# Optimization experiments

Hardware: AMD Instinct MI355X
Metric: run time of the kernel (lower is better)

Reference implementation:

```python
import jax, jax.numpy as jnp
import numpy as np

N_NODES, N_EDGES, D, H, G = 50000, 800000, 128, 128, 2048
EPS_BN = 1e-5


def _bn(x, g, b, m, v):
    # inference-mode BatchNorm1d
    return (x - m) * jax.lax.rsqrt(v + EPS_BN) * g + b


def _gin_mlp(h, w1, b1, g1, be1, m1, v1, w2, b2, g2, be2, m2, v2):
    h = jax.nn.relu(_bn(h @ w1 + b1, g1, be1, m1, v1))
    return jax.nn.relu(_bn(h @ w2 + b2, g2, be2, m2, v2))


def _gin(x, src, dst, *mlp_params):
    # GINConv with eps=0: MLP(x_i + sum_{j->i} x_j)
    agg = jax.ops.segment_sum(x[src], dst, num_segments=x.shape[0])
    return _gin_mlp(x + agg, *mlp_params)


def setup_inputs() -> dict:
    key = jax.random.key(0)
    ks = jax.random.split(key, 16)
    inp = {
        'x': jax.random.normal(ks[0], (N_NODES, D), dtype=jnp.float32),
        'edge_index': jax.random.randint(ks[1], (2, N_EDGES), 0, N_NODES, dtype=jnp.int64),
        'batch': jnp.sort(jax.random.randint(ks[2], (N_NODES,), 0, G, dtype=jnp.int64)),
    }
    def lin(k, fin, fout):
        return jax.random.normal(k, (fin, fout), dtype=jnp.float32) * (1.0 / np.sqrt(fin))
    # conv1 MLP
    inp.update(w11=lin(ks[3], D, H), b11=jnp.zeros((H,)), g11=jnp.ones((H,)), be11=jnp.zeros((H,)), m11=jnp.zeros((H,)), v11=jnp.ones((H,)))
    inp.update(w12=lin(ks[4], H, H), b12=jnp.zeros((H,)), g12=jnp.ones((H,)), be12=jnp.zeros((H,)), m12=jnp.zeros((H,)), v12=jnp.ones((H,)))
    # conv2 MLP
    inp.update(w21=lin(ks[5], H, H), b21=jnp.zeros((H,)), g21=jnp.ones((H,)), be21=jnp.zeros((H,)), m21=jnp.zeros((H,)), v21=jnp.ones((H,)))
    inp.update(w22=lin(ks[6], H, H), b22=jnp.zeros((H,)), g22=jnp.ones((H,)), be22=jnp.zeros((H,)), m22=jnp.zeros((H,)), v22=jnp.ones((H,)))
    # classifier
    inp.update(wc1=lin(ks[7], H, 64), bc1=jnp.zeros((64,)), gc1=jnp.ones((64,)), bec1=jnp.zeros((64,)), mc1=jnp.zeros((64,)), vc1=jnp.ones((64,)))
    inp.update(wc2=lin(ks[8], 64, 2), bc2=jnp.zeros((2,)))
    return inp


def reference(x, edge_index, batch,
              w11, b11, g11, be11, m11, v11, w12, b12, g12, be12, m12, v12,
              w21, b21, g21, be21, m21, v21, w22, b22, g22, be22, m22, v22,
              wc1, bc1, gc1, bec1, mc1, vc1, wc2, bc2):
    src, dst = edge_index[0], edge_index[1]
    out1 = _gin(x, src, dst, w11, b11, g11, be11, m11, v11, w12, b12, g12, be12, m12, v12)
    # F.relu on already-ReLU'd output is a no-op but kept for fidelity
    out1 = jax.nn.relu(out1)
    out2 = _gin(out1, src, dst, w21, b21, g21, be21, m21, v21, w22, b22, g22, be22, m22, v22)
    out2 = jax.nn.relu(out2)
    # global mean pool over graph ids
    sums = jax.ops.segment_sum(out2, batch, num_segments=G)
    cnt = jax.ops.segment_sum(jnp.ones((out2.shape[0],), out2.dtype), batch, num_segments=G)
    pooled = sums / jnp.maximum(cnt, 1.0)[:, None]
    # classifier (dropout = identity in eval)
    h = jax.nn.relu(_bn(pooled @ wc1 + bc1, gc1, bec1, mc1, vc1))
    logits = h @ wc2 + bc2
    return logits
```

## Files before the change

### kernel.cpp

```cpp
#include <hip/hip_runtime.h>

#define NN 50000
#define NE 800000
#define DD 128
#define GG 2048
#define EPS 1e-5f
#define NBUK 196
#define CHUNK 4096
#define CAP 5120
#define CVTB 3125

typedef __attribute__((ext_vector_type(8))) short short8;
typedef __attribute__((ext_vector_type(4))) float floatx4;

__device__ __forceinline__ ushort f2b(float f) {
  uint u = __float_as_uint(f);
  uint r = ((u >> 16) & 1u) + 0x7fffu;
  return (ushort)((u + r) >> 16);
}
__device__ __forceinline__ float b2f(ushort h) {
  return __uint_as_float(((uint)h) << 16);
}
__device__ __forceinline__ float blo(uint u) { return __uint_as_float(u << 16); }
__device__ __forceinline__ float bhi(uint u) { return __uint_as_float(u & 0xffff0000u); }

__global__ __launch_bounds__(256) void k_pre(
    const float* __restrict__ W11, const float* __restrict__ W12,
    const float* __restrict__ W21, const float* __restrict__ W22,
    const float* __restrict__ b11, const float* __restrict__ g11,
    const float* __restrict__ be11, const float* __restrict__ m11,
    const float* __restrict__ v11,
    const float* __restrict__ b12, const float* __restrict__ g12,
    const float* __restrict__ be12, const float* __restrict__ m12,
    const float* __restrict__ v12,
    const float* __restrict__ b21, const float* __restrict__ g21,
    const float* __restrict__ be21, const float* __restrict__ m21,
    const float* __restrict__ v21,
    const float* __restrict__ b22, const float* __restrict__ g22,
    const float* __restrict__ be22, const float* __restrict__ m22,
    const float* __restrict__ v22,
    ushort* __restrict__ Wb, float* __restrict__ albb,
    int* __restrict__ buk_cnt) {
  int t = threadIdx.x;
  int b = blockIdx.x;
  if (b == 64) {
    buk_cnt[t] = 0;
    if (t < DD) {
      float a;
      a = g11[t] * rsqrtf(v11[t] + EPS);
      albb[0 * DD + t] = a;
      albb[1 * DD + t] = (b11[t] - m11[t]) * a + be11[t];
      a = g12[t] * rsqrtf(v12[t] + EPS);
      albb[2 * DD + t] = a;
      albb[3 * DD + t] = (b12[t] - m12[t]) * a + be12[t];
      a = g21[t] * rsqrtf(v21[t] + EPS);
      albb[4 * DD + t] = a;
      albb[5 * DD + t] = (b21[t] - m21[t]) * a + be21[t];
      a = g22[t] * rsqrtf(v22[t] + EPS);
      albb[6 * DD + t] = a;
      albb[7 * DD + t] = (b22[t] - m22[t]) * a + be22[t];
    }
    return;
  }
  const float* Ws[4] = {W11, W12, W21, W22};
  int widx = b >> 4;
  int idx = (b & 15) * 256 + t;
  int c = idx >> 5;
  int k0 = (idx & 31) * 4;
  const float* W = Ws[widx];
  ushort4 p;
  p.x = f2b(W[(k0 + 0) * DD + c]);
  p.y = f2b(W[(k0 + 1) * DD + c]);
  p.z = f2b(W[(k0 + 2) * DD + c]);
  p.w = f2b(W[(k0 + 3) * DD + c]);
  *(ushort4*)&Wb[(size_t)widx * DD * DD + c * DD + (k0 ^ ((c & 7) << 3))] = p;
}

__global__ __launch_bounds__(256) void k_binC(const float4* __restrict__ x,
                                              short8* __restrict__ xb,
                                              const int* __restrict__ ei,
                                              int* __restrict__ buk_cnt,
                                              uint* __restrict__ buk_pairs) {
  __shared__ int hist[256];
  __shared__ int gbase[256];
  __shared__ int lcur[256];
  int t = threadIdx.x;
  if (blockIdx.x < CVTB) {
    int i = blockIdx.x * 256 + t;
    float4 a = x[2 * i], c = x[2 * i + 1];
    short8 v;
    v[0] = (short)f2b(a.x); v[1] = (short)f2b(a.y);
    v[2] = (short)f2b(a.z); v[3] = (short)f2b(a.w);
    v[4] = (short)f2b(c.x); v[5] = (short)f2b(c.y);
    v[6] = (short)f2b(c.z); v[7] = (short)f2b(c.w);
    xb[i] = v;
    return;
  }
  int blk = blockIdx.x - CVTB;
  int e0 = blk * CHUNK;
  int nE = min(CHUNK, NE - e0);
  hist[t] = 0;
  lcur[t] = 0;
  gbase[t] = 0;
  __syncthreads();
  uint pk[16];
#pragma unroll
  for (int i = 0; i < 16; ++i) {
    int off = i * 256 + t;
    if (off < nE) {
      int e = e0 + off;
      int s = ei[e], d = ei[NE + e];
      int b = d >> 8;
      pk[i] = ((uint)b << 24) | ((uint)(d & 255) << 16) | (uint)s;
      atomicAdd(&hist[b], 1);
    } else {
      pk[i] = 0xffffffffu;
    }
  }
  __syncthreads();
  if (t < NBUK && hist[t] > 0) gbase[t] = atomicAdd(&buk_cnt[t], hist[t]);
  __syncthreads();
#pragma unroll
  for (int i = 0; i < 16; ++i) {
    if (pk[i] != 0xffffffffu) {
      int b = pk[i] >> 24;
      int lo = atomicAdd(&lcur[b], 1);
      int off = gbase[b] + lo;
      if (off < CAP) buk_pairs[(size_t)b * CAP + off] = pk[i];
    }
  }
}

__global__ __launch_bounds__(256) void k_bfill(const uint* __restrict__ buk_pairs,
                                               const int* __restrict__ buk_cnt,
                                               int* __restrict__ row_ptr,
                                               int* __restrict__ csr_src) {
  __shared__ int sc[256];
  __shared__ int deg[256];
  __shared__ int pos[256];
  int b = blockIdx.x, t = threadIdx.x;
  int c = (t < NBUK) ? min(buk_cnt[t], CAP) : 0;
  sc[t] = c;
  __syncthreads();
  int s1 = c;
  for (int off = 1; off < 256; off <<= 1) {
    int o = (t >= off) ? sc[t - off] : 0;
    __syncthreads();
    s1 += o;
    sc[t] = s1;
    __syncthreads();
  }
  int beg = (b == 0) ? 0 : sc[b - 1];
  int cnt = sc[b] - beg;
  const uint* src = buk_pairs + (size_t)b * CAP;
  deg[t] = 0;
  __syncthreads();
  for (int i = t; i < cnt; i += 256) {
    atomicAdd(&deg[(src[i] >> 16) & 255], 1);
  }
  __syncthreads();
  int d = deg[t];
  int sum = d;
  pos[t] = sum;
  __syncthreads();
  for (int off = 1; off < 256; off <<= 1) {
    int o = (t >= off) ? pos[t - off] : 0;
    __syncthreads();
    sum += o;
    pos[t] = sum;
    __syncthreads();
  }
  int myStart = beg + sum - d;
  int node = b * 256 + t;
  if (node < NN) row_ptr[node] = myStart;
  if (node == NN - 1) row_ptr[NN] = NE;
  __syncthreads();
  pos[t] = myStart;
  __syncthreads();
  for (int i = t; i < cnt; i += 256) {
    uint p = src[i];
    int lo = atomicAdd(&pos[(p >> 16) & 255], 1);
    csr_src[lo] = (int)(p & 0xffffu);
  }
}

__global__ __launch_bounds__(256) void k_agg(const uint* __restrict__ X,
                                             const int* __restrict__ row_ptr,
                                             const int* __restrict__ csr_src,
                                             uint* __restrict__ out) {
  int node = (blockIdx.x * 256 + threadIdx.x) >> 6;
  if (node >= NN) return;
  int lane = threadIdx.x & 63;
  uint s0 = X[(size_t)node * 64 + lane];
  float ax = blo(s0), ay = bhi(s0);
  int beg = row_ptr[node], end = row_ptr[node + 1];
  for (int i = beg; i < end; i += 64) {
    int idx = i + lane;
    int my = (idx < end) ? __builtin_nontemporal_load(csr_src + idx) : 0;
    int cnt = min(64, end - i);
    int j = 0;
    for (; j + 8 <= cnt; j += 8) {
      int n0 = __shfl(my, j + 0);
      int n1 = __shfl(my, j + 1);
      int n2 = __shfl(my, j + 2);
      int n3 = __shfl(my, j + 3);
      int n4 = __shfl(my, j + 4);
      int n5 = __shfl(my, j + 5);
      int n6 = __shfl(my, j + 6);
      int n7 = __shfl(my, j + 7);
      uint v0 = X[(size_t)n0 * 64 + lane];
      uint v1 = X[(size_t)n1 * 64 + lane];
      uint v2 = X[(size_t)n2 * 64 + lane];
      uint v3 = X[(size_t)n3 * 64 + lane];
      uint v4 = X[(size_t)n4 * 64 + lane];
      uint v5 = X[(size_t)n5 * 64 + lane];
      uint v6 = X[(size_t)n6 * 64 + lane];
      uint v7 = X[(size_t)n7 * 64 + lane];
      ax += blo(v0); ay += bhi(v0);
      ax += blo(v1); ay += bhi(v1);
      ax += blo(v2); ay += bhi(v2);
      ax += blo(v3); ay += bhi(v3);
      ax += blo(v4); ay += bhi(v4);
      ax += blo(v5); ay += bhi(v5);
      ax += blo(v6); ay += bhi(v6);
      ax += blo(v7); ay += bhi(v7);
    }
    for (; j + 4 <= cnt; j += 4) {
      int n0 = __shfl(my, j + 0);
      int n1 = __shfl(my, j + 1);
      int n2 = __shfl(my, j + 2);
      int n3 = __shfl(my, j + 3);
      uint v0 = X[(size_t)n0 * 64 + lane];
      uint v1 = X[(size_t)n1 * 64 + lane];
      uint v2 = X[(size_t)n2 * 64 + lane];
      uint v3 = X[(size_t)n3 * 64 + lane];
      ax += blo(v0); ay += bhi(v0);
      ax += blo(v1); ay += bhi(v1);
      ax += blo(v2); ay += bhi(v2);
      ax += blo(v3); ay += bhi(v3);
    }
    for (; j < cnt; ++j) {
      int s = __shfl(my, j);
      uint v = X[(size_t)s * 64 + lane];
      ax += blo(v);
      ay += bhi(v);
    }
  }
  out[(size_t)node * 64 + lane] = (uint)f2b(ax) | ((uint)f2b(ay) << 16);
}

__global__ __launch_bounds__(256) void k_mlp(const ushort* __restrict__ A,
                                             const ushort* __restrict__ Wb1,
                                             const ushort* __restrict__ Wb2,
                                             const float* __restrict__ albb,
                                             ushort* __restrict__ out) {
  __shared__ ushort Wt[DD * DD];
  __shared__ ushort mid[64 * DD];
  __shared__ float al1[DD], bb1[DD], al2[DD], bb2[DD];
  int t = threadIdx.x;
  for (int ii = t; ii < 2048; ii += 256) ((short8*)Wt)[ii] = ((const short8*)Wb1)[ii];
  if (t < DD) {
    al1[t] = albb[0 * DD + t];
    bb1[t] = albb[1 * DD + t];
    al2[t] = albb[2 * DD + t];
    bb2[t] = albb[3 * DD + t];
  }
  int w = t >> 6, l = t & 63;
  int lr = l & 15, lg = l >> 4;
  int rowBase = blockIdx.x * 64 + w * 16;
  int arow = min(rowBase + lr, NN - 1);
  const short8* Ar = (const short8*)(A + (size_t)arow * DD);
  short8 a0 = Ar[0 * 4 + lg];
  short8 a1 = Ar[1 * 4 + lg];
  short8 a2 = Ar[2 * 4 + lg];
  short8 a3 = Ar[3 * 4 + lg];
  __syncthreads();

  int mrowb = w * 16;
#pragma unroll
  for (int ct = 0; ct < 8; ++ct) {
    int c = ct * 16 + lr;
    int sw = (c & 7) << 3;
    const ushort* wr = Wt + c * DD;
    short8 b0 = *(const short8*)(wr + ((0 * 32 + lg * 8) ^ sw));
    short8 b1 = *(const short8*)(wr + ((1 * 32 + lg * 8) ^ sw));
    short8 b2 = *(const short8*)(wr + ((2 * 32 + lg * 8) ^ sw));
    short8 b3 = *(const short8*)(wr + ((3 * 32 + lg * 8) ^ sw));
    floatx4 acc = {0.f, 0.f, 0.f, 0.f};
    acc = __builtin_amdgcn_mfma_f32_16x16x32_bf16(a0, b0, acc, 0, 0, 0);
    acc = __builtin_amdgcn_mfma_f32_16x16x32_bf16(a1, b1, acc, 0, 0, 0);
    acc = __builtin_amdgcn_mfma_f32_16x16x32_bf16(a2, b2, acc, 0, 0, 0);
    acc = __builtin_amdgcn_mfma_f32_16x16x32_bf16(a3, b3, acc, 0, 0, 0);
    float alc = al1[c], bbc = bb1[c];
#pragma unroll
    for (int reg = 0; reg < 4; ++reg) {
      int row = mrowb + lg * 4 + reg;
      mid[row * DD + (c ^ ((row & 7) << 3))] = f2b(fmaxf(acc[reg] * alc + bbc, 0.f));
    }
  }
  __syncthreads();

  int mr = mrowb + lr;
  int msw = (mr & 7) << 3;
  const ushort* mrp = mid + mr * DD;
  short8 c0 = *(const short8*)(mrp + ((0 * 32 + lg * 8) ^ msw));
  short8 c1 = *(const short8*)(mrp + ((1 * 32 + lg * 8) ^ msw));
  short8 c2 = *(const short8*)(mrp + ((2 * 32 + lg * 8) ^ msw));
  short8 c3 = *(const short8*)(mrp + ((3 * 32 + lg * 8) ^ msw));
  for (int ii = t; ii < 2048; ii += 256) ((short8*)Wt)[ii] = ((const short8*)Wb2)[ii];
  __syncthreads();

#pragma unroll
  for (int ct = 0; ct < 8; ++ct) {
    int c = ct * 16 + lr;
    int sw = (c & 7) << 3;
    const ushort* wr = Wt + c * DD;
    short8 b0 = *(const short8*)(wr + ((0 * 32 + lg * 8) ^ sw));
    short8 b1 = *(const short8*)(wr + ((1 * 32 + lg * 8) ^ sw));
    short8 b2 = *(const short8*)(wr + ((2 * 32 + lg * 8) ^ sw));
    short8 b3 = *(const short8*)(wr + ((3 * 32 + lg * 8) ^ sw));
    floatx4 acc = {0.f, 0.f, 0.f, 0.f};
    acc = __builtin_amdgcn_mfma_f32_16x16x32_bf16(c0, b0, acc, 0, 0, 0);
    acc = __builtin_amdgcn_mfma_f32_16x16x32_bf16(c1, b1, acc, 0, 0, 0);
    acc = __builtin_amdgcn_mfma_f32_16x16x32_bf16(c2, b2, acc, 0, 0, 0);
    acc = __builtin_amdgcn_mfma_f32_16x16x32_bf16(c3, b3, acc, 0, 0, 0);
    float alc = al2[c], bbc = bb2[c];
#pragma unroll
    for (int reg = 0; reg < 4; ++reg) {
      int r = rowBase + lg * 4 + reg;
      if (r < NN) {
        out[(size_t)r * DD + c] = f2b(fmaxf(acc[reg] * alc + bbc, 0.f));
      }
    }
  }
}

__device__ __forceinline__ int lb(const int* __restrict__ a, int n, int v) {
  int lo = 0, hi = n;
  while (lo < hi) {
    int mid = (lo + hi) >> 1;
    if (a[mid] < v) lo = mid + 1;
    else hi = mid;
  }
  return lo;
}

__global__ __launch_bounds__(128) void k_poolcls(const ushort* __restrict__ h,
                                                 const int* __restrict__ batch,
                                                 const float* __restrict__ wc1,
                                                 const float* __restrict__ bc1,
                                                 const float* __restrict__ gc1,
                                                 const float* __restrict__ bec1,
                                                 const float* __restrict__ mc1,
                                                 const float* __restrict__ vc1,
                                                 const float* __restrict__ wc2,
                                                 const float* __restrict__ bc2,
                                                 float* __restrict__ outp) {
  __shared__ int sb[2];
  __shared__ float ps[DD];
  __shared__ float hh[64];
  int g = blockIdx.x, t = threadIdx.x;
  if (t < 2) sb[t] = lb(batch, NN, g + t);
  __syncthreads();
  int beg = sb[0], end = sb[1];
  float acc = 0.f;
  int n = beg;
  for (; n + 4 <= end; n += 4) {
    float x0 = b2f(h[(size_t)(n + 0) * DD + t]);
    float x1 = b2f(h[(size_t)(n + 1) * DD + t]);
    float x2 = b2f(h[(size_t)(n + 2) * DD + t]);
    float x3 = b2f(h[(size_t)(n + 3) * DD + t]);
    acc += x0 + x1 + x2 + x3;
  }
  for (; n < end; ++n) acc += b2f(h[(size_t)n * DD + t]);
  float inv = 1.0f / fmaxf((float)(end - beg), 1.0f);
  ps[t] = acc * inv;
  __syncthreads();
  if (t < 64) {
    float a2 = 0.f;
#pragma unroll 8
    for (int k = 0; k < DD; ++k) a2 += ps[k] * wc1[k * 64 + t];
    float a = gc1[t] * rsqrtf(vc1[t] + EPS);
    float b2 = (bc1[t] - mc1[t]) * a + bec1[t];
    hh[t] = fmaxf(a2 * a + b2, 0.f);
  }
  __syncthreads();
  if (t < 2) {
    float a2 = bc2[t];
#pragma unroll
    for (int k = 0; k < 64; ++k) a2 += hh[k] * wc2[k * 2 + t];
    outp[g * 2 + t] = a2;
  }
}

extern "C" void kernel_launch(void* const* d_in, const int* in_sizes, int n_in,
                              void* d_out, int out_size, void* d_ws, size_t ws_size,
                              hipStream_t stream) {
  const float* x = (const float*)d_in[0];
  const int* ei = (const int*)d_in[1];
  const int* batch = (const int*)d_in[2];
  const float* w11 = (const float*)d_in[3];
  const float* b11 = (const float*)d_in[4];
  const float* g11 = (const float*)d_in[5];
  const float* be11 = (const float*)d_in[6];
  const float* m11 = (const float*)d_in[7];
  const float* v11 = (const float*)d_in[8];
  const float* w12 = (const float*)d_in[9];
  const float* b12 = (const float*)d_in[10];
  const float* g12 = (const float*)d_in[11];
  const float* be12 = (const float*)d_in[12];
  const float* m12 = (const float*)d_in[13];
  const float* v12 = (const float*)d_in[14];
  const float* w21 = (const float*)d_in[15];
  const float* b21 = (const float*)d_in[16];
  const float* g21 = (const float*)d_in[17];
  const float* be21 = (const float*)d_in[18];
  const float* m21 = (const float*)d_in[19];
  const float* v21 = (const float*)d_in[20];
  const float* w22 = (const float*)d_in[21];
  const float* b22 = (const float*)d_in[22];
  const float* g22 = (const float*)d_in[23];
  const float* be22 = (const float*)d_in[24];
  const float* m22 = (const float*)d_in[25];
  const float* v22 = (const float*)d_in[26];
  const float* wc1 = (const float*)d_in[27];
  const float* bc1 = (const float*)d_in[28];
  const float* gc1 = (const float*)d_in[29];
  const float* bec1 = (const float*)d_in[30];
  const float* mc1 = (const float*)d_in[31];
  const float* vc1 = (const float*)d_in[32];
  const float* wc2 = (const float*)d_in[33];
  const float* bc2 = (const float*)d_in[34];

  const size_t NB = (size_t)NN * DD;
  ushort* XB = (ushort*)d_ws;
  ushort* AG = XB + NB;
  ushort* H1 = AG + NB;
  ushort* H2 = H1 + NB;
  int* row_ptr = (int*)(H2 + NB);
  int* buk_cnt = row_ptr + NN + 1;
  int* buk_base = buk_cnt + 256;
  int* csr_src = buk_base + 256;
  uint* buk_pairs = (uint*)(csr_src + NE);
  ushort* Wb = (ushort*)(buk_pairs + (size_t)NBUK * CAP);
  float* albb = (float*)(Wb + 4 * DD * DD);

  const int gemmBlocks = (NN + 63) / 64;
  const int aggBlocks = NN * 64 / 256;

  k_pre<<<65, 256, 0, stream>>>(w11, w12, w21, w22,
                                b11, g11, be11, m11, v11,
                                b12, g12, be12, m12, v12,
                                b21, g21, be21, m21, v21,
                                b22, g22, be22, m22, v22,
                                Wb, albb, buk_cnt);
  k_binC<<<CVTB + NBUK, 256, 0, stream>>>((const float4*)x, (short8*)XB, ei,
                                          buk_cnt, buk_pairs);
  k_bfill<<<NBUK, 256, 0, stream>>>(buk_pairs, buk_cnt, row_ptr, csr_src);

  k_agg<<<aggBlocks, 256, 0, stream>>>((const uint*)XB, row_ptr, csr_src, (uint*)AG);
  k_mlp<<<gemmBlocks, 256, 0, stream>>>(AG, Wb, Wb + DD * DD, albb, H1);

  k_agg<<<aggBlocks, 256, 0, stream>>>((const uint*)H1, row_ptr, csr_src, (uint*)AG);
  k_mlp<<<gemmBlocks, 256, 0, stream>>>(AG, Wb + 2 * DD * DD, Wb + 3 * DD * DD,
                                        albb + 4 * DD, H2);

  k_poolcls<<<GG, 128, 0, stream>>>(H2, batch, wc1, bc1, gc1, bec1, mc1, vc1,
                                    wc2, bc2, (float*)d_out);
}
```

Before: 150.1 us.

## Fuse neighbor aggregation into the GIN MLP kernel via shared memory

The separate aggregation kernel is merged into the MLP kernel. Each wave now gathers and sums the neighbor features for its 16 rows, one row at a time, and writes the bf16 results into the swizzled shared tile that feeds the MFMA GEMMs. This removes the intermediate AG buffer write and read plus one launch per layer. In exchange, each wave handles its 16 nodes serially, so there is less memory-level parallelism per wave during the gather. Latency hiding now depends on occupancy, which the kernel's large shared-memory footprint limits.

```diff
diff --git a/kernel.cpp b/kernel.cpp
--- a/kernel.cpp
+++ b/kernel.cpp
@@ -184,76 +184,13 @@
   }
 }
 
-__global__ __launch_bounds__(256) void k_agg(const uint* __restrict__ X,
-                                             const int* __restrict__ row_ptr,
-                                             const int* __restrict__ csr_src,
-                                             uint* __restrict__ out) {
-  int node = (blockIdx.x * 256 + threadIdx.x) >> 6;
-  if (node >= NN) return;
-  int lane = threadIdx.x & 63;
-  uint s0 = X[(size_t)node * 64 + lane];
-  float ax = blo(s0), ay = bhi(s0);
-  int beg = row_ptr[node], end = row_ptr[node + 1];
-  for (int i = beg; i < end; i += 64) {
-    int idx = i + lane;
-    int my = (idx < end) ? __builtin_nontemporal_load(csr_src + idx) : 0;
-    int cnt = min(64, end - i);
-    int j = 0;
-    for (; j + 8 <= cnt; j += 8) {
-      int n0 = __shfl(my, j + 0);
-      int n1 = __shfl(my, j + 1);
-      int n2 = __shfl(my, j + 2);
-      int n3 = __shfl(my, j + 3);
-      int n4 = __shfl(my, j + 4);
-      int n5 = __shfl(my, j + 5);
-      int n6 = __shfl(my, j + 6);
-      int n7 = __shfl(my, j + 7);
-      uint v0 = X[(size_t)n0 * 64 + lane];
-      uint v1 = X[(size_t)n1 * 64 + lane];
-      uint v2 = X[(size_t)n2 * 64 + lane];
-      uint v3 = X[(size_t)n3 * 64 + lane];
-      uint v4 = X[(size_t)n4 * 64 + lane];
-      uint v5 = X[(size_t)n5 * 64 + lane];
-      uint v6 = X[(size_t)n6 * 64 + lane];
-      uint v7 = X[(size_t)n7 * 64 + lane];
-      ax += blo(v0); ay += bhi(v0);
-      ax += blo(v1); ay += bhi(v1);
-      ax += blo(v2); ay += bhi(v2);
-      ax += blo(v3); ay += bhi(v3);
-      ax += blo(v4); ay += bhi(v4);
-      ax += blo(v5); ay += bhi(v5);
-      ax += blo(v6); ay += bhi(v6);
-      ax += blo(v7); ay += bhi(v7);
-    }
-    for (; j + 4 <= cnt; j += 4) {
-      int n0 = __shfl(my, j + 0);
-      int n1 = __shfl(my, j + 1);
-      int n2 = __shfl(my, j + 2);
-      int n3 = __shfl(my, j + 3);
-      uint v0 = X[(size_t)n0 * 64 + lane];
-      uint v1 = X[(size_t)n1 * 64 + lane];
-      uint v2 = X[(size_t)n2 * 64 + lane];
-      uint v3 = X[(size_t)n3 * 64 + lane];
-      ax += blo(v0); ay += bhi(v0);
-      ax += blo(v1); ay += bhi(v1);
-      ax += blo(v2); ay += bhi(v2);
-      ax += blo(v3); ay += bhi(v3);
-    }
-    for (; j < cnt; ++j) {
-      int s = __shfl(my, j);
-      uint v = X[(size_t)s * 64 + lane];
-      ax += blo(v);
-      ay += bhi(v);
-    }
-  }
-  out[(size_t)node * 64 + lane] = (uint)f2b(ax) | ((uint)f2b(ay) << 16);
-}
-
-__global__ __launch_bounds__(256) void k_mlp(const ushort* __restrict__ A,
-                                             const ushort* __restrict__ Wb1,
-                                             const ushort* __restrict__ Wb2,
-                                             const float* __restrict__ albb,
-                                             ushort* __restrict__ out) {
+__global__ __launch_bounds__(256) void k_fmlp(const uint* __restrict__ X,
+                                              const int* __restrict__ row_ptr,
+                                              const int* __restrict__ csr_src,
+                                              const ushort* __restrict__ Wb1,
+                                              const ushort* __restrict__ Wb2,
+                                              const float* __restrict__ albb,
+                                              ushort* __restrict__ out) {
   __shared__ ushort Wt[DD * DD];
   __shared__ ushort mid[64 * DD];
   __shared__ float al1[DD], bb1[DD], al2[DD], bb2[DD];
@@ -268,13 +205,77 @@
   int w = t >> 6, l = t & 63;
   int lr = l & 15, lg = l >> 4;
   int rowBase = blockIdx.x * 64 + w * 16;
-  int arow = min(rowBase + lr, NN - 1);
-  const short8* Ar = (const short8*)(A + (size_t)arow * DD);
-  short8 a0 = Ar[0 * 4 + lg];
-  short8 a1 = Ar[1 * 4 + lg];
-  short8 a2 = Ar[2 * 4 + lg];
-  short8 a3 = Ar[3 * 4 + lg];
-  __syncthreads();
+  uint* midu = (uint*)mid;
+
+  for (int r = 0; r < 16; ++r) {
+    int nd = min(rowBase + r, NN - 1);
+    uint s0 = X[(size_t)nd * 64 + l];
+    float ax = blo(s0), ay = bhi(s0);
+    int beg = row_ptr[nd], end = row_ptr[nd + 1];
+    for (int i = beg; i < end; i += 64) {
+      int idx = i + l;
+      int my = (idx < end) ? __builtin_nontemporal_load(csr_src + idx) : 0;
+      int cnt = min(64, end - i);
+      int j = 0;
+      for (; j + 8 <= cnt; j += 8) {
+        int n0 = __shfl(my, j + 0);
+        int n1 = __shfl(my, j + 1);
+        int n2 = __shfl(my, j + 2);
+        int n3 = __shfl(my, j + 3);
+        int n4 = __shfl(my, j + 4);
+        int n5 = __shfl(my, j + 5);
+        int n6 = __shfl(my, j + 6);
+        int n7 = __shfl(my, j + 7);
+        uint v0 = X[(size_t)n0 * 64 + l];
+        uint v1 = X[(size_t)n1 * 64 + l];
+        uint v2 = X[(size_t)n2 * 64 + l];
+        uint v3 = X[(size_t)n3 * 64 + l];
+        uint v4 = X[(size_t)n4 * 64 + l];
+        uint v5 = X[(size_t)n5 * 64 + l];
+        uint v6 = X[(size_t)n6 * 64 + l];
+        uint v7 = X[(size_t)n7 * 64 + l];
+        ax += blo(v0); ay += bhi(v0);
+        ax += blo(v1); ay += bhi(v1);
+        ax += blo(v2); ay += bhi(v2);
+        ax += blo(v3); ay += bhi(v3);
+        ax += blo(v4); ay += bhi(v4);
+        ax += blo(v5); ay += bhi(v5);
+        ax += blo(v6); ay += bhi(v6);
+        ax += blo(v7); ay += bhi(v7);
+      }
+      for (; j + 4 <= cnt; j += 4) {
+        int n0 = __shfl(my, j + 0);
+        int n1 = __shfl(my, j + 1);
+        int n2 = __shfl(my, j + 2);
+        int n3 = __shfl(my, j + 3);
+        uint v0 = X[(size_t)n0 * 64 + l];
+        uint v1 = X[(size_t)n1 * 64 + l];
+        uint v2 = X[(size_t)n2 * 64 + l];
+        uint v3 = X[(size_t)n3 * 64 + l];
+        ax += blo(v0); ay += bhi(v0);
+        ax += blo(v1); ay += bhi(v1);
+        ax += blo(v2); ay += bhi(v2);
+        ax += blo(v3); ay += bhi(v3);
+      }
+      for (; j < cnt; ++j) {
+        int s = __shfl(my, j);
+        uint v = X[(size_t)s * 64 + l];
+        ax += blo(v);
+        ay += bhi(v);
+      }
+    }
+    int mrow = w * 16 + r;
+    midu[mrow * 64 + (l ^ ((mrow & 7) << 2))] = (uint)f2b(ax) | ((uint)f2b(ay) << 16);
+  }
+  __syncthreads();
+
+  int mr = w * 16 + lr;
+  int msw = (mr & 7) << 3;
+  const ushort* mrp = mid + mr * DD;
+  short8 a0 = *(const short8*)(mrp + ((0 * 32 + lg * 8) ^ msw));
+  short8 a1 = *(const short8*)(mrp + ((1 * 32 + lg * 8) ^ msw));
+  short8 a2 = *(const short8*)(mrp + ((2 * 32 + lg * 8) ^ msw));
+  short8 a3 = *(const short8*)(mrp + ((3 * 32 + lg * 8) ^ msw));
 
   int mrowb = w * 16;
 #pragma unroll
@@ -300,9 +301,6 @@
   }
   __syncthreads();
 
-  int mr = mrowb + lr;
-  int msw = (mr & 7) << 3;
-  const ushort* mrp = mid + mr * DD;
   short8 c0 = *(const short8*)(mrp + ((0 * 32 + lg * 8) ^ msw));
   short8 c1 = *(const short8*)(mrp + ((1 * 32 + lg * 8) ^ msw));
   short8 c2 = *(const short8*)(mrp + ((2 * 32 + lg * 8) ^ msw));
@@ -327,9 +325,11 @@
     float alc = al2[c], bbc = bb2[c];
 #pragma unroll
     for (int reg = 0; reg < 4; ++reg) {
-      int r = rowBase + lg * 4 + reg;
-      if (r < NN) {
-        out[(size_t)r * DD + c] = f2b(fmaxf(acc[reg] * alc + bbc, 0.f));
+      int r = rowBase - w * 16 + w * 16 + lg * 4 + reg;
+      int rr = rowBase + lg * 4 + reg;
+      (void)r;
+      if (rr < NN) {
+        out[(size_t)rr * DD + c] = f2b(fmaxf(acc[reg] * alc + bbc, 0.f));
       }
     }
   }
@@ -434,8 +434,7 @@
 
   const size_t NB = (size_t)NN * DD;
   ushort* XB = (ushort*)d_ws;
-  ushort* AG = XB + NB;
-  ushort* H1 = AG + NB;
+  ushort* H1 = XB + NB;
   ushort* H2 = H1 + NB;
   int* row_ptr = (int*)(H2 + NB);
   int* buk_cnt = row_ptr + NN + 1;
@@ -446,7 +445,6 @@
   float* albb = (float*)(Wb + 4 * DD * DD);
 
   const int gemmBlocks = (NN + 63) / 64;
-  const int aggBlocks = NN * 64 / 256;
 
   k_pre<<<65, 256, 0, stream>>>(w11, w12, w21, w22,
                                 b11, g11, be11, m11, v11,
@@ -458,12 +456,12 @@
                                           buk_cnt, buk_pairs);
   k_bfill<<<NBUK, 256, 0, stream>>>(buk_pairs, buk_cnt, row_ptr, csr_src);
 
-  k_agg<<<aggBlocks, 256, 0, stream>>>((const uint*)XB, row_ptr, csr_src, (uint*)AG);
-  k_mlp<<<gemmBlocks, 256, 0, stream>>>(AG, Wb, Wb + DD * DD, albb, H1);
-
-  k_agg<<<aggBlocks, 256, 0, stream>>>((const uint*)H1, row_ptr, csr_src, (uint*)AG);
-  k_mlp<<<gemmBlocks, 256, 0, stream>>>(AG, Wb + 2 * DD * DD, Wb + 3 * DD * DD,
-                                        albb + 4 * DD, H2);
+  k_fmlp<<<gemmBlocks, 256, 0, stream>>>((const uint*)XB, row_ptr, csr_src,
+                                         Wb, Wb + DD * DD, albb, H1);
+
+  k_fmlp<<<gemmBlocks, 256, 0, stream>>>((const uint*)H1, row_ptr, csr_src,
+                                         Wb + 2 * DD * DD, Wb + 3 * DD * DD,
+                                         albb + 4 * DD, H2);
 
   k_poolcls<<<GG, 128, 0, stream>>>(H2, batch, wc1, bc1, gc1, bec1, mc1, vc1,
                                     wc2, bc2, (float*)d_out);
```

Result: slower. 232.7 us (+55.0%).
